# Optimization experiments

Hardware: AMD Instinct MI355X
Metric: run time of the kernel (lower is better)

Reference implementation:

```python
import jax, jax.numpy as jnp
import numpy as np


def setup_inputs() -> dict:
    key = jax.random.key(0)
    k1, k2 = jax.random.split(key)
    N = 2_000_000
    rotation = jax.random.normal(k1, (N, 3, 3), dtype=jnp.float32)
    # learned parameter: eye(3) + 0.001 * randn(3,3)
    mat = jnp.eye(3, dtype=jnp.float32) + 0.001 * jax.random.normal(k2, (3, 3), dtype=jnp.float32)
    return {"rotation": rotation, "mat": mat}


def reference(rotation, mat):
    # new_mat[n] = rotation[n] @ mat   (mat broadcast over the batch)
    new_mat = jnp.einsum('nab,bc->nac', rotation, mat)
    # batched 3x3 SVD; polar orthogonal factor U @ V^T
    U, S, Vh = jnp.linalg.svd(new_mat, full_matrices=False)
    out = jnp.einsum('nab,nbc->nac', U, Vh)  # Vh is already V^T
    logdet = jnp.zeros((rotation.shape[0],), dtype=rotation.dtype)
    return out, logdet
```

## Files before the change

### kernel.cpp

```cpp
#include <hip/hip_runtime.h>
#include <math.h>

typedef float v2f __attribute__((ext_vector_type(2)));

constexpr int BLOCK = 256;

__global__ __launch_bounds__(BLOCK) void polar3x3_kernel(
    const float* __restrict__ rot,
    const float* __restrict__ mat,
    float* __restrict__ outq,
    float* __restrict__ logdet,
    int N)
{
    const long long tid = (long long)blockIdx.x * BLOCK + threadIdx.x;
    const long long i0 = tid * 2;
    if (i0 >= N) return;
    const bool full = (i0 + 1 < N);

    float X[18];
    if (full) {
        const v2f* rp2 = (const v2f*)(rot + i0 * 9);
        #pragma unroll
        for (int k = 0; k < 9; ++k) { v2f w = rp2[k]; X[2*k] = w.x; X[2*k+1] = w.y; }
    } else {
        const float* rp = rot + i0 * 9;
        #pragma unroll
        for (int k = 0; k < 9; ++k) X[k] = rp[k];
        #pragma unroll
        for (int k = 9; k < 18; ++k) X[k] = 0.f;
        X[9] = X[13] = X[17] = 1.f;
    }

    const float m0=mat[0], m1=mat[1], m2=mat[2], m3=mat[3], m4=mat[4],
                m5=mat[5], m6=mat[6], m7=mat[7], m8=mat[8];
    const double dM = (double)m0*((double)m4*m8-(double)m5*m7)
                    - (double)m1*((double)m3*m8-(double)m5*m6)
                    + (double)m2*((double)m3*m7-(double)m4*m6);

    float detA[2];
    #pragma unroll
    for (int j = 0; j < 2; ++j) {
        float* p = &X[9*j];
        const float r0=p[0],r1=p[1],r2=p[2],r3=p[3],r4=p[4],r5=p[5],r6=p[6],r7=p[7],r8=p[8];
        const double dR = (double)r0*((double)r4*r8-(double)r5*r7)
                        - (double)r1*((double)r3*r8-(double)r5*r6)
                        + (double)r2*((double)r3*r7-(double)r4*r6);
        detA[j] = (float)(dR * dM);
        p[0]=fmaf(r0,m0,fmaf(r1,m3,r2*m6));
        p[1]=fmaf(r0,m1,fmaf(r1,m4,r2*m7));
        p[2]=fmaf(r0,m2,fmaf(r1,m5,r2*m8));
        p[3]=fmaf(r3,m0,fmaf(r4,m3,r5*m6));
        p[4]=fmaf(r3,m1,fmaf(r4,m4,r5*m7));
        p[5]=fmaf(r3,m2,fmaf(r4,m5,r5*m8));
        p[6]=fmaf(r6,m0,fmaf(r7,m3,r8*m6));
        p[7]=fmaf(r6,m1,fmaf(r7,m4,r8*m7));
        p[8]=fmaf(r6,m2,fmaf(r7,m5,r8*m8));
    }

    #pragma unroll
    for (int it = 0; it < 5; ++it) {
        #pragma unroll
        for (int j = 0; j < 2; ++j) {
            float* p = &X[9*j];
            const float x0=p[0],x1=p[1],x2=p[2],x3=p[3],x4=p[4],x5=p[5],x6=p[6],x7=p[7],x8=p[8];
            const float c0=fmaf(x4,x8,-x5*x7), c1=fmaf(x5,x6,-x3*x8), c2=fmaf(x3,x7,-x4*x6);
            const float c3=fmaf(x2,x7,-x1*x8), c4=fmaf(x0,x8,-x2*x6), c5=fmaf(x1,x6,-x0*x7);
            const float c6=fmaf(x1,x5,-x2*x4), c7=fmaf(x2,x3,-x0*x5), c8=fmaf(x0,x4,-x1*x3);
            const float det = (it==0) ? detA[j] : fmaf(x0,c0,fmaf(x1,c1,x2*c2));
            const float adet = fmaxf(fabsf(det), 1e-30f);
            float nX2, nC2;
            { const float a=fmaf(x1,x1,x0*x0), b=fmaf(x3,x3,x2*x2),
                          e=fmaf(x5,x5,x4*x4), d=fmaf(x7,x7,x6*x6);
              nX2=(a+b)+(e+fmaf(x8,x8,d)); }
            { const float a=fmaf(c1,c1,c0*c0), b=fmaf(c3,c3,c2*c2),
                          e=fmaf(c5,c5,c4*c4), d=fmaf(c7,c7,c6*c6);
              nC2=(a+b)+(e+fmaf(c8,c8,d)); }
            const float h  = __builtin_amdgcn_rsqf(adet);
            const float pr = __builtin_amdgcn_sqrtf(__builtin_amdgcn_sqrtf(
                                 nC2*__builtin_amdgcn_rcpf(nX2)));
            const float qr = __builtin_amdgcn_sqrtf(__builtin_amdgcn_sqrtf(
                                 nX2*__builtin_amdgcn_rcpf(nC2)));
            const float s = 0.5f*pr*h;
            const float t = copysignf(0.5f*qr*h, det);
            p[0]=fmaf(s,x0,t*c0); p[1]=fmaf(s,x1,t*c1); p[2]=fmaf(s,x2,t*c2);
            p[3]=fmaf(s,x3,t*c3); p[4]=fmaf(s,x4,t*c4); p[5]=fmaf(s,x5,t*c5);
            p[6]=fmaf(s,x6,t*c6); p[7]=fmaf(s,x7,t*c7); p[8]=fmaf(s,x8,t*c8);
        }
    }

    #pragma unroll
    for (int j = 0; j < 2; ++j) {
        float* p = &X[9*j];
        const float x0=p[0],x1=p[1],x2=p[2],x3=p[3],x4=p[4],x5=p[5],x6=p[6],x7=p[7],x8=p[8];
        const float c0=fmaf(x4,x8,-x5*x7), c1=fmaf(x5,x6,-x3*x8), c2=fmaf(x3,x7,-x4*x6);
        const float c3=fmaf(x2,x7,-x1*x8), c4=fmaf(x0,x8,-x2*x6), c5=fmaf(x1,x6,-x0*x7);
        const float c6=fmaf(x1,x5,-x2*x4), c7=fmaf(x2,x3,-x0*x5), c8=fmaf(x0,x4,-x1*x3);
        const float det = fmaf(x0,c0,fmaf(x1,c1,x2*c2));
        const float t = 0.5f*__builtin_amdgcn_rcpf(det);
        p[0]=fmaf(0.5f,x0,t*c0); p[1]=fmaf(0.5f,x1,t*c1); p[2]=fmaf(0.5f,x2,t*c2);
        p[3]=fmaf(0.5f,x3,t*c3); p[4]=fmaf(0.5f,x4,t*c4); p[5]=fmaf(0.5f,x5,t*c5);
        p[6]=fmaf(0.5f,x6,t*c6); p[7]=fmaf(0.5f,x7,t*c7); p[8]=fmaf(0.5f,x8,t*c8);
    }

    float* op = outq + i0 * 9;
    if (full) {
        v2f* op2 = (v2f*)op;
        #pragma unroll
        for (int k = 0; k < 9; ++k) {
            v2f w; w.x = X[2*k]; w.y = X[2*k+1];
            op2[k] = w;
        }
        v2f z; z.x = 0.f; z.y = 0.f;
        *(v2f*)(logdet + i0) = z;
    } else {
        #pragma unroll
        for (int k = 0; k < 9; ++k) op[k] = X[k];
        logdet[i0] = 0.f;
    }
}

extern "C" void kernel_launch(void* const* d_in, const int* in_sizes, int n_in,
                              void* d_out, int out_size, void* d_ws, size_t ws_size,
                              hipStream_t stream) {
    const float* rot = (const float*)d_in[0];
    const float* mat = (const float*)d_in[1];
    float* out = (float*)d_out;
    const int N = in_sizes[0] / 9;
    float* logdet = out + (long long)N * 9;
    const long long nthreads = (N + 1) / 2;
    const int nblocks = (int)((nthreads + BLOCK - 1) / BLOCK);
    polar3x3_kernel<<<nblocks, BLOCK, 0, stream>>>(rot, mat, out, logdet, N);
}
```

Before: 146.0 us.

## Stage matrices through LDS for coalesced float4 loads and stores, one matrix per thread

Each block now cooperatively copies its 256 matrices from global memory into shared memory with float4 accesses. Each thread then reads its own 3x3 matrix from LDS, runs the polar iteration, writes the result back to LDS, and the block stores the result with coalesced float4 writes. This replaces the strided 8-byte per-thread accesses with fully coalesced 16-byte transactions, and it drops from two matrices per thread to one, which doubles the number of threads. The cost is two barriers, LDS traffic with 9-float stride bank conflicts, and less per-thread ILP.

Result: faster. 138.8 us (-4.9%).

```diff
diff --git a/kernel.cpp b/kernel.cpp
--- a/kernel.cpp
+++ b/kernel.cpp
@@ -1,7 +1,5 @@
 #include <hip/hip_runtime.h>
 #include <math.h>
-
-typedef float v2f __attribute__((ext_vector_type(2)));
 
 constexpr int BLOCK = 256;
 
@@ -12,23 +10,20 @@
     float* __restrict__ logdet,
     int N)
 {
-    const long long tid = (long long)blockIdx.x * BLOCK + threadIdx.x;
-    const long long i0 = tid * 2;
-    if (i0 >= N) return;
-    const bool full = (i0 + 1 < N);
+    __shared__ float lds[BLOCK * 9];
+    const int tid = threadIdx.x;
+    const long long base = (long long)blockIdx.x * BLOCK;
+    const int rem = (int)(N - base);
+    const int nmat = rem < BLOCK ? rem : BLOCK;
+    const int nflt = nmat * 9;
+    const int nv4 = nflt >> 2;
 
-    float X[18];
-    if (full) {
-        const v2f* rp2 = (const v2f*)(rot + i0 * 9);
-        #pragma unroll
-        for (int k = 0; k < 9; ++k) { v2f w = rp2[k]; X[2*k] = w.x; X[2*k+1] = w.y; }
-    } else {
-        const float* rp = rot + i0 * 9;
-        #pragma unroll
-        for (int k = 0; k < 9; ++k) X[k] = rp[k];
-        #pragma unroll
-        for (int k = 9; k < 18; ++k) X[k] = 0.f;
-        X[9] = X[13] = X[17] = 1.f;
+    const float* gsrc = rot + base * 9;
+    {
+        const float4* g4 = (const float4*)gsrc;
+        float4* l4 = (float4*)lds;
+        for (int i = tid; i < nv4; i += BLOCK) l4[i] = g4[i];
+        for (int i = (nv4 << 2) + tid; i < nflt; i += BLOCK) lds[i] = gsrc[i];
     }
 
     const float m0=mat[0], m1=mat[1], m2=mat[2], m3=mat[3], m4=mat[4],
@@ -36,87 +31,82 @@
     const double dM = (double)m0*((double)m4*m8-(double)m5*m7)
                     - (double)m1*((double)m3*m8-(double)m5*m6)
                     + (double)m2*((double)m3*m7-(double)m4*m6);
+    __syncthreads();
 
-    float detA[2];
-    #pragma unroll
-    for (int j = 0; j < 2; ++j) {
-        float* p = &X[9*j];
-        const float r0=p[0],r1=p[1],r2=p[2],r3=p[3],r4=p[4],r5=p[5],r6=p[6],r7=p[7],r8=p[8];
+    const bool active = tid < nmat;
+    float x0=1.f,x1=0.f,x2=0.f,x3=0.f,x4=1.f,x5=0.f,x6=0.f,x7=0.f,x8=1.f;
+    float detA = 1.f;
+
+    if (active) {
+        const float* r = &lds[tid * 9];
+        const float r0=r[0],r1=r[1],r2=r[2],r3=r[3],r4=r[4],r5=r[5],r6=r[6],r7=r[7],r8=r[8];
         const double dR = (double)r0*((double)r4*r8-(double)r5*r7)
                         - (double)r1*((double)r3*r8-(double)r5*r6)
                         + (double)r2*((double)r3*r7-(double)r4*r6);
-        detA[j] = (float)(dR * dM);
-        p[0]=fmaf(r0,m0,fmaf(r1,m3,r2*m6));
-        p[1]=fmaf(r0,m1,fmaf(r1,m4,r2*m7));
-        p[2]=fmaf(r0,m2,fmaf(r1,m5,r2*m8));
-        p[3]=fmaf(r3,m0,fmaf(r4,m3,r5*m6));
-        p[4]=fmaf(r3,m1,fmaf(r4,m4,r5*m7));
-        p[5]=fmaf(r3,m2,fmaf(r4,m5,r5*m8));
-        p[6]=fmaf(r6,m0,fmaf(r7,m3,r8*m6));
-        p[7]=fmaf(r6,m1,fmaf(r7,m4,r8*m7));
-        p[8]=fmaf(r6,m2,fmaf(r7,m5,r8*m8));
+        detA = (float)(dR * dM);
+        x0=fmaf(r0,m0,fmaf(r1,m3,r2*m6));
+        x1=fmaf(r0,m1,fmaf(r1,m4,r2*m7));
+        x2=fmaf(r0,m2,fmaf(r1,m5,r2*m8));
+        x3=fmaf(r3,m0,fmaf(r4,m3,r5*m6));
+        x4=fmaf(r3,m1,fmaf(r4,m4,r5*m7));
+        x5=fmaf(r3,m2,fmaf(r4,m5,r5*m8));
+        x6=fmaf(r6,m0,fmaf(r7,m3,r8*m6));
+        x7=fmaf(r6,m1,fmaf(r7,m4,r8*m7));
+        x8=fmaf(r6,m2,fmaf(r7,m5,r8*m8));
     }
 
     #pragma unroll
     for (int it = 0; it < 5; ++it) {
-        #pragma unroll
-        for (int j = 0; j < 2; ++j) {
-            float* p = &X[9*j];
-            const float x0=p[0],x1=p[1],x2=p[2],x3=p[3],x4=p[4],x5=p[5],x6=p[6],x7=p[7],x8=p[8];
-            const float c0=fmaf(x4,x8,-x5*x7), c1=fmaf(x5,x6,-x3*x8), c2=fmaf(x3,x7,-x4*x6);
-            const float c3=fmaf(x2,x7,-x1*x8), c4=fmaf(x0,x8,-x2*x6), c5=fmaf(x1,x6,-x0*x7);
-            const float c6=fmaf(x1,x5,-x2*x4), c7=fmaf(x2,x3,-x0*x5), c8=fmaf(x0,x4,-x1*x3);
-            const float det = (it==0) ? detA[j] : fmaf(x0,c0,fmaf(x1,c1,x2*c2));
-            const float adet = fmaxf(fabsf(det), 1e-30f);
-            float nX2, nC2;
-            { const float a=fmaf(x1,x1,x0*x0), b=fmaf(x3,x3,x2*x2),
-                          e=fmaf(x5,x5,x4*x4), d=fmaf(x7,x7,x6*x6);
-              nX2=(a+b)+(e+fmaf(x8,x8,d)); }
-            { const float a=fmaf(c1,c1,c0*c0), b=fmaf(c3,c3,c2*c2),
-                          e=fmaf(c5,c5,c4*c4), d=fmaf(c7,c7,c6*c6);
-              nC2=(a+b)+(e+fmaf(c8,c8,d)); }
-            const float h  = __builtin_amdgcn_rsqf(adet);
-            const float pr = __builtin_amdgcn_sqrtf(__builtin_amdgcn_sqrtf(
-                                 nC2*__builtin_amdgcn_rcpf(nX2)));
-            const float qr = __builtin_amdgcn_sqrtf(__builtin_amdgcn_sqrtf(
-                                 nX2*__builtin_amdgcn_rcpf(nC2)));
-            const float s = 0.5f*pr*h;
-            const float t = copysignf(0.5f*qr*h, det);
-            p[0]=fmaf(s,x0,t*c0); p[1]=fmaf(s,x1,t*c1); p[2]=fmaf(s,x2,t*c2);
-            p[3]=fmaf(s,x3,t*c3); p[4]=fmaf(s,x4,t*c4); p[5]=fmaf(s,x5,t*c5);
-            p[6]=fmaf(s,x6,t*c6); p[7]=fmaf(s,x7,t*c7); p[8]=fmaf(s,x8,t*c8);
-        }
+        const float c0=fmaf(x4,x8,-x5*x7), c1=fmaf(x5,x6,-x3*x8), c2=fmaf(x3,x7,-x4*x6);
+        const float c3=fmaf(x2,x7,-x1*x8), c4=fmaf(x0,x8,-x2*x6), c5=fmaf(x1,x6,-x0*x7);
+        const float c6=fmaf(x1,x5,-x2*x4), c7=fmaf(x2,x3,-x0*x5), c8=fmaf(x0,x4,-x1*x3);
+        const float det = (it==0) ? detA : fmaf(x0,c0,fmaf(x1,c1,x2*c2));
+        const float adet = fmaxf(fabsf(det), 1e-30f);
+        float nX2, nC2;
+        { const float a=fmaf(x1,x1,x0*x0), b=fmaf(x3,x3,x2*x2),
+                      e=fmaf(x5,x5,x4*x4), d=fmaf(x7,x7,x6*x6);
+          nX2=(a+b)+(e+fmaf(x8,x8,d)); }
+        { const float a=fmaf(c1,c1,c0*c0), b=fmaf(c3,c3,c2*c2),
+                      e=fmaf(c5,c5,c4*c4), d=fmaf(c7,c7,c6*c6);
+          nC2=(a+b)+(e+fmaf(c8,c8,d)); }
+        const float h  = __builtin_amdgcn_rsqf(adet);
+        const float pr = __builtin_amdgcn_sqrtf(__builtin_amdgcn_sqrtf(
+                             nC2*__builtin_amdgcn_rcpf(nX2)));
+        const float qr = __builtin_amdgcn_sqrtf(__builtin_amdgcn_sqrtf(
+                             nX2*__builtin_amdgcn_rcpf(nC2)));
+        const float s = 0.5f*pr*h;
+        const float t = copysignf(0.5f*qr*h, det);
+        x0=fmaf(s,x0,t*c0); x1=fmaf(s,x1,t*c1); x2=fmaf(s,x2,t*c2);
+        x3=fmaf(s,x3,t*c3); x4=fmaf(s,x4,t*c4); x5=fmaf(s,x5,t*c5);
+        x6=fmaf(s,x6,t*c6); x7=fmaf(s,x7,t*c7); x8=fmaf(s,x8,t*c8);
     }
-
-    #pragma unroll
-    for (int j = 0; j < 2; ++j) {
-        float* p = &X[9*j];
-        const float x0=p[0],x1=p[1],x2=p[2],x3=p[3],x4=p[4],x5=p[5],x6=p[6],x7=p[7],x8=p[8];
+    {
         const float c0=fmaf(x4,x8,-x5*x7), c1=fmaf(x5,x6,-x3*x8), c2=fmaf(x3,x7,-x4*x6);
         const float c3=fmaf(x2,x7,-x1*x8), c4=fmaf(x0,x8,-x2*x6), c5=fmaf(x1,x6,-x0*x7);
         const float c6=fmaf(x1,x5,-x2*x4), c7=fmaf(x2,x3,-x0*x5), c8=fmaf(x0,x4,-x1*x3);
         const float det = fmaf(x0,c0,fmaf(x1,c1,x2*c2));
         const float t = 0.5f*__builtin_amdgcn_rcpf(det);
-        p[0]=fmaf(0.5f,x0,t*c0); p[1]=fmaf(0.5f,x1,t*c1); p[2]=fmaf(0.5f,x2,t*c2);
-        p[3]=fmaf(0.5f,x3,t*c3); p[4]=fmaf(0.5f,x4,t*c4); p[5]=fmaf(0.5f,x5,t*c5);
-        p[6]=fmaf(0.5f,x6,t*c6); p[7]=fmaf(0.5f,x7,t*c7); p[8]=fmaf(0.5f,x8,t*c8);
+        x0=fmaf(0.5f,x0,t*c0); x1=fmaf(0.5f,x1,t*c1); x2=fmaf(0.5f,x2,t*c2);
+        x3=fmaf(0.5f,x3,t*c3); x4=fmaf(0.5f,x4,t*c4); x5=fmaf(0.5f,x5,t*c5);
+        x6=fmaf(0.5f,x6,t*c6); x7=fmaf(0.5f,x7,t*c7); x8=fmaf(0.5f,x8,t*c8);
     }
 
-    float* op = outq + i0 * 9;
-    if (full) {
-        v2f* op2 = (v2f*)op;
-        #pragma unroll
-        for (int k = 0; k < 9; ++k) {
-            v2f w; w.x = X[2*k]; w.y = X[2*k+1];
-            op2[k] = w;
-        }
-        v2f z; z.x = 0.f; z.y = 0.f;
-        *(v2f*)(logdet + i0) = z;
-    } else {
-        #pragma unroll
-        for (int k = 0; k < 9; ++k) op[k] = X[k];
-        logdet[i0] = 0.f;
+    if (active) {
+        float* w = &lds[tid * 9];
+        w[0]=x0; w[1]=x1; w[2]=x2; w[3]=x3; w[4]=x4;
+        w[5]=x5; w[6]=x6; w[7]=x7; w[8]=x8;
     }
+    __syncthreads();
+
+    float* gdst = outq + base * 9;
+    {
+        float4* g4 = (float4*)gdst;
+        const float4* l4 = (const float4*)lds;
+        for (int i = tid; i < nv4; i += BLOCK) g4[i] = l4[i];
+        for (int i = (nv4 << 2) + tid; i < nflt; i += BLOCK) gdst[i] = lds[i];
+    }
+
+    if (base + tid < N) logdet[base + tid] = 0.0f;
 }
 
 extern "C" void kernel_launch(void* const* d_in, const int* in_sizes, int n_in,
@@ -127,7 +117,6 @@
     float* out = (float*)d_out;
     const int N = in_sizes[0] / 9;
     float* logdet = out + (long long)N * 9;
-    const long long nthreads = (N + 1) / 2;
-    const int nblocks = (int)((nthreads + BLOCK - 1) / BLOCK);
+    const int nblocks = (N + BLOCK - 1) / BLOCK;
     polar3x3_kernel<<<nblocks, BLOCK, 0, stream>>>(rot, mat, out, logdet, N);
 }
```
